# Kernel optimization log

Measured on AMD Instinct MI355X. Metric: run time of the kernel, lower is better.

Reference implementation:

```python
import jax, jax.numpy as jnp
import numpy as np

B = 131072

def _lin(x, w, b):
    return x @ w.T + b

def setup_inputs() -> dict:
    key = jax.random.key(0)
    ks = jax.random.split(key, 32)
    def rn(k, shape, scale=0.05):
        return jax.random.normal(k, shape, dtype=jnp.float32) * scale
    inp = {
        "x": rn(ks[0], (B, 256), 1.0),
        "w": rn(ks[1], (B, 36), 1.0),
        "h0": rn(ks[2], (B, 32), 1.0),
        "c0": rn(ks[3], (B, 32), 1.0),
        "fc1_w": rn(ks[4], (128, 256)), "fc1_b": rn(ks[5], (128,)),
        "fc1a_w": rn(ks[6], (128, 164)), "fc1a_b": rn(ks[7], (128,)),
        "fc1b_w": rn(ks[8], (128, 128)), "fc1b_b": rn(ks[9], (128,)),
        "w_game": rn(ks[10], (1, 12), 1.0),
        "fc1c_w": rn(ks[11], (64, 140)), "fc1c_b": rn(ks[12], (64,)),
        "fc2_w": rn(ks[13], (32, 64)), "fc2_b": rn(ks[14], (32,)),
        "fc3_w": rn(ks[15], (32, 32)), "fc3_b": rn(ks[16], (32,)),
        "w_ih": rn(ks[17], (128, 32)), "w_hh": rn(ks[18], (128, 32)),
        "b_ih": rn(ks[19], (128,)), "b_hh": rn(ks[20], (128,)),
        "fc4_w": rn(ks[21], (32, 32)), "fc4_b": rn(ks[22], (32,)),
        "fc5_w": rn(ks[23], (1, 32)), "fc5_b": rn(ks[24], (1,)),
    }
    return inp

def reference(x, w, h0, c0, fc1_w, fc1_b, fc1a_w, fc1a_b, fc1b_w, fc1b_b,
              w_game, fc1c_w, fc1c_b, fc2_w, fc2_b, fc3_w, fc3_b,
              w_ih, w_hh, b_ih, b_hh, fc4_w, fc4_b, fc5_w, fc5_b):
    b = x.shape[0]
    h = jax.nn.relu(_lin(x, fc1_w, fc1_b))                      # [B,128]
    h = jnp.concatenate([h, w], axis=-1)                        # [B,164]
    h = jax.nn.relu(_lin(h, fc1a_w, fc1a_b))                    # [B,128]
    h = jax.nn.relu(_lin(h, fc1b_w, fc1b_b))                    # [B,128]
    wg = jnp.broadcast_to(w_game.reshape(1, 12), (b, 12))
    h = jnp.concatenate([h, wg], axis=-1)                       # [B,140]
    h = jax.nn.relu(_lin(h, fc1c_w, fc1c_b))                    # [B,64]
    h = jax.nn.relu(_lin(h, fc2_w, fc2_b))                      # [B,32]
    h = jax.nn.relu(_lin(h, fc3_w, fc3_b))                      # [B,32]
    # LSTMCell step (torch gate order: input, forget, cell, output)
    gates = _lin(h, w_ih, b_ih) + _lin(h0, w_hh, b_hh)          # [B,128]
    i_g, f_g, g_g, o_g = jnp.split(gates, 4, axis=-1)
    c_new = jax.nn.sigmoid(f_g) * c0 + jax.nn.sigmoid(i_g) * jnp.tanh(g_g)
    h_new = jax.nn.sigmoid(o_g) * jnp.tanh(c_new)               # [B,32]
    out = jax.nn.relu(_lin(h_new, fc4_w, fc4_b))                # [B,32]
    out = _lin(out, fc5_w, fc5_b)                               # [B,1]
    return jax.nn.sigmoid(out)
```

## Files before the change

kernel.cpp:

```cpp
#include <hip/hip_runtime.h>
#include <hip/hip_bf16.h>


typedef __bf16 bf16x8 __attribute__((ext_vector_type(8)));
typedef float  f32x4  __attribute__((ext_vector_type(4)));
typedef int    i32x4  __attribute__((ext_vector_type(4)));

#define MFMA16(A, B, C) __builtin_amdgcn_mfma_f32_16x16x32_bf16((A), (B), (C), 0, 0, 0)

#define WOFF_FC1    0
#define WOFF_FC1A_H 32768
#define WOFF_FC1B   49152
#define WOFF_FC1C   65536
#define LDS_ELEMS   73728
#define WOFF_FC1A_W 73728
#define WOFF_FC2    81920
#define WOFF_FC3    83968
#define WOFF_WIH    84992
#define WOFF_WHH    89088
#define WOFF_FC4    93184
#define WTOT        94208
#define BOFF_FC1  0
#define BOFF_FC1A 128
#define BOFF_FC1B 256
#define BOFF_FC1C 384
#define BOFF_FC2  448
#define BOFF_FC3  480
#define BOFF_LSTM 512
#define BOFF_FC4  640
#define BTOT      672

__device__ __forceinline__ void conv_frag(int rel, const float* __restrict__ src,
                                          __bf16* __restrict__ dst,
                                          int ns, int Krow, int kbase, int klim, int perm) {
    int j    = rel & 7;
    int lane = (rel >> 3) & 63;
    int fs   = rel >> 9;
    int s    = fs % ns;
    int t    = fs / ns;
    int gq   = lane >> 4;
    int n    = 16 * t + (lane & 15);
    int k    = perm ? (16 * (2 * s + (j >> 2)) + 4 * gq + (j & 3))
                    : (32 * s + 8 * gq + j);
    float v  = (k < klim) ? src[n * Krow + kbase + k] : 0.f;
    dst[rel] = (__bf16)v;
}

__global__ void prep_kernel(const float* __restrict__ fc1w,  const float* __restrict__ fc1b,
                            const float* __restrict__ fc1aw, const float* __restrict__ fc1ab,
                            const float* __restrict__ fc1bw, const float* __restrict__ fc1bb,
                            const float* __restrict__ wgame, const float* __restrict__ fc1cw,
                            const float* __restrict__ fc1cb, const float* __restrict__ fc2w,
                            const float* __restrict__ fc2b,  const float* __restrict__ fc3w,
                            const float* __restrict__ fc3b,  const float* __restrict__ wih,
                            const float* __restrict__ whh,   const float* __restrict__ bih,
                            const float* __restrict__ bhh,   const float* __restrict__ fc4w,
                            const float* __restrict__ fc4b,
                            __bf16* __restrict__ wsw, float* __restrict__ wsb) {
    int idx = blockIdx.x * 256 + threadIdx.x;
    if (idx < WTOT) {
        if      (idx < WOFF_FC1A_H) conv_frag(idx - WOFF_FC1,    fc1w,  wsw + WOFF_FC1,    8, 256,   0, 256, 0);
        else if (idx < WOFF_FC1B)   conv_frag(idx - WOFF_FC1A_H, fc1aw, wsw + WOFF_FC1A_H, 4, 164,   0, 128, 1);
        else if (idx < WOFF_FC1C)   conv_frag(idx - WOFF_FC1B,   fc1bw, wsw + WOFF_FC1B,   4, 128,   0, 128, 1);
        else if (idx < WOFF_FC1A_W) conv_frag(idx - WOFF_FC1C,   fc1cw, wsw + WOFF_FC1C,   4, 140,   0, 128, 1);
        else if (idx < WOFF_FC2)    conv_frag(idx - WOFF_FC1A_W, fc1aw, wsw + WOFF_FC1A_W, 2, 164, 128,  36, 0);
        else if (idx < WOFF_FC3)    conv_frag(idx - WOFF_FC2,    fc2w,  wsw + WOFF_FC2,    2,  64,   0,  64, 1);
        else if (idx < WOFF_WIH)    conv_frag(idx - WOFF_FC3,    fc3w,  wsw + WOFF_FC3,    1,  32,   0,  32, 1);
        else if (idx < WOFF_WHH)    conv_frag(idx - WOFF_WIH,    wih,   wsw + WOFF_WIH,    1,  32,   0,  32, 1);
        else if (idx < WOFF_FC4)    conv_frag(idx - WOFF_WHH,    whh,   wsw + WOFF_WHH,    1,  32,   0,  32, 0);
        else                        conv_frag(idx - WOFF_FC4,    fc4w,  wsw + WOFF_FC4,    1,  32,   0,  32, 1);
    } else if (idx < WTOT + BTOT) {
        int bi = idx - WTOT;
        float v;
        if      (bi < 128) v = fc1b[bi];
        else if (bi < 256) v = fc1ab[bi - 128];
        else if (bi < 384) v = fc1bb[bi - 256];
        else if (bi < 448) {
            int n = bi - 384;
            v = fc1cb[n];
            for (int q = 0; q < 12; ++q) v += fc1cw[n * 140 + 128 + q] * wgame[q];
        }
        else if (bi < 480) v = fc2b[bi - 448];
        else if (bi < 512) v = fc3b[bi - 480];
        else if (bi < 640) { int n = bi - 512; v = bih[n] + bhh[n]; }
        else               v = fc4b[bi - 640];
        wsb[bi] = v;
    }
}

__device__ __forceinline__ bf16x8 ld8f(const float* __restrict__ p) {
    f32x4 a = *(const f32x4*)p;
    f32x4 b = *(const f32x4*)(p + 4);
    bf16x8 r;
    r[0] = (__bf16)a[0]; r[1] = (__bf16)a[1]; r[2] = (__bf16)a[2]; r[3] = (__bf16)a[3];
    r[4] = (__bf16)b[0]; r[5] = (__bf16)b[1]; r[6] = (__bf16)b[2]; r[7] = (__bf16)b[3];
    return r;
}

__device__ __forceinline__ bf16x8 ld4f_masked(const float* __restrict__ p, bool on) {
    f32x4 v = {0.f, 0.f, 0.f, 0.f};
    if (on) v = *(const f32x4*)p;
    bf16x8 r;
    r[0] = (__bf16)v[0]; r[1] = (__bf16)v[1]; r[2] = (__bf16)v[2]; r[3] = (__bf16)v[3];
    r[4] = (__bf16)0.f;  r[5] = (__bf16)0.f;  r[6] = (__bf16)0.f;  r[7] = (__bf16)0.f;
    return r;
}

__device__ __forceinline__ bf16x8 packrelu(const f32x4* a, int s) {
    bf16x8 r;
#pragma unroll
    for (int j = 0; j < 8; ++j) {
        float v = a[2 * s + (j >> 2)][j & 3];
        r[j] = (__bf16)fmaxf(v, 0.f);
    }
    return r;
}

__device__ __forceinline__ float sigm(float v)  { return 1.f / (1.f + __expf(-v)); }
__device__ __forceinline__ float tanh_(float v) { return 1.f - 2.f / (1.f + __expf(2.f * v)); }

__global__ __launch_bounds__(512, 2) void fused_mlp_lstm(
        const float* __restrict__ x,  const float* __restrict__ w,
        const float* __restrict__ h0, const float* __restrict__ c0,
        const float* __restrict__ fc5w, const float* __restrict__ fc5b,
        const __bf16* __restrict__ wsw, const float* __restrict__ wsb,
        float* __restrict__ out) {
    __shared__ __align__(16) __bf16 slds[LDS_ELEMS];

    const int tid     = threadIdx.x;
    const int lane    = tid & 63;
    const int wv      = blockIdx.x * 8 + (tid >> 6);
    const int gq      = lane >> 4;
    const int mr      = lane & 15;
    const int rowbase = wv * 32;
    const int row0    = rowbase + mr;
    const int row1    = rowbase + 16 + mr;

    {
        const i32x4* gs = (const i32x4*)wsw;
        i32x4*       sd = (i32x4*)slds;
#pragma unroll
        for (int i = 0; i < 18; ++i) sd[i * 512 + tid] = gs[i * 512 + tid];
    }

    bf16x8 xf[2][8];
#pragma unroll
    for (int s = 0; s < 8; ++s) {
        xf[0][s] = ld8f(x + row0 * 256 + 32 * s + 8 * gq);
        xf[1][s] = ld8f(x + row1 * 256 + 32 * s + 8 * gq);
    }
    bf16x8 wxa0 = ld8f(w + row0 * 36 + 8 * gq);
    bf16x8 wxb0 = ld8f(w + row1 * 36 + 8 * gq);
    bf16x8 wxa1 = ld4f_masked(w + row0 * 36 + 32, gq == 0);
    bf16x8 wxb1 = ld4f_masked(w + row1 * 36 + 32, gq == 0);

    __syncthreads();

    const bf16x8* Wfc1  = (const bf16x8*)(slds + WOFF_FC1);
    const bf16x8* Wf1aH = (const bf16x8*)(slds + WOFF_FC1A_H);
    const bf16x8* Wfc1b = (const bf16x8*)(slds + WOFF_FC1B);
    const bf16x8* Wfc1c = (const bf16x8*)(slds + WOFF_FC1C);
    const bf16x8* Wf1aW = (const bf16x8*)(wsw + WOFF_FC1A_W);
    const bf16x8* Wfc2  = (const bf16x8*)(wsw + WOFF_FC2);
    const bf16x8* Wfc3  = (const bf16x8*)(wsw + WOFF_FC3);
    const bf16x8* Wwih  = (const bf16x8*)(wsw + WOFF_WIH);
    const bf16x8* Wwhh  = (const bf16x8*)(wsw + WOFF_WHH);
    const bf16x8* Wfc4  = (const bf16x8*)(wsw + WOFF_FC4);

    f32x4 acc1[2][8];
#pragma unroll
    for (int t = 0; t < 8; ++t) {
        f32x4 bv = *(const f32x4*)(wsb + BOFF_FC1 + 16 * t + 4 * gq);
        acc1[0][t] = bv; acc1[1][t] = bv;
    }
#pragma unroll
    for (int s = 0; s < 8; ++s) {
#pragma unroll
        for (int t = 0; t < 8; ++t) {
            bf16x8 wf = Wfc1[(t * 8 + s) * 64 + lane];
            acc1[0][t] = MFMA16(wf, xf[0][s], acc1[0][t]);
            acc1[1][t] = MFMA16(wf, xf[1][s], acc1[1][t]);
        }
    }
    bf16x8 h0fa = ld8f(h0 + row0 * 32 + 8 * gq);
    bf16x8 h0fb = ld8f(h0 + row1 * 32 + 8 * gq);

    bf16x8 h1f[2][4];
#pragma unroll
    for (int s = 0; s < 4; ++s) { h1f[0][s] = packrelu(acc1[0], s); h1f[1][s] = packrelu(acc1[1], s); }

    f32x4 acc2[2][8];
#pragma unroll
    for (int t = 0; t < 8; ++t) {
        f32x4 bv = *(const f32x4*)(wsb + BOFF_FC1A + 16 * t + 4 * gq);
        acc2[0][t] = bv; acc2[1][t] = bv;
    }
#pragma unroll
    for (int s = 0; s < 4; ++s) {
#pragma unroll
        for (int t = 0; t < 8; ++t) {
            bf16x8 wf = Wf1aH[(t * 4 + s) * 64 + lane];
            acc2[0][t] = MFMA16(wf, h1f[0][s], acc2[0][t]);
            acc2[1][t] = MFMA16(wf, h1f[1][s], acc2[1][t]);
        }
    }
#pragma unroll
    for (int t = 0; t < 8; ++t) {
        bf16x8 wf0 = Wf1aW[(t * 2 + 0) * 64 + lane];
        bf16x8 wf1 = Wf1aW[(t * 2 + 1) * 64 + lane];
        acc2[0][t] = MFMA16(wf0, wxa0, acc2[0][t]);
        acc2[1][t] = MFMA16(wf0, wxb0, acc2[1][t]);
        acc2[0][t] = MFMA16(wf1, wxa1, acc2[0][t]);
        acc2[1][t] = MFMA16(wf1, wxb1, acc2[1][t]);
    }
    f32x4 c0r[2][2];
#pragma unroll
    for (int t2 = 0; t2 < 2; ++t2) {
        c0r[0][t2] = *(const f32x4*)(c0 + row0 * 32 + 16 * t2 + 4 * gq);
        c0r[1][t2] = *(const f32x4*)(c0 + row1 * 32 + 16 * t2 + 4 * gq);
    }

    bf16x8 h2f[2][4];
#pragma unroll
    for (int s = 0; s < 4; ++s) { h2f[0][s] = packrelu(acc2[0], s); h2f[1][s] = packrelu(acc2[1], s); }

    f32x4 acc3[2][8];
#pragma unroll
    for (int t = 0; t < 8; ++t) {
        f32x4 bv = *(const f32x4*)(wsb + BOFF_FC1B + 16 * t + 4 * gq);
        acc3[0][t] = bv; acc3[1][t] = bv;
    }
#pragma unroll
    for (int s = 0; s < 4; ++s) {
#pragma unroll
        for (int t = 0; t < 8; ++t) {
            bf16x8 wf = Wfc1b[(t * 4 + s) * 64 + lane];
            acc3[0][t] = MFMA16(wf, h2f[0][s], acc3[0][t]);
            acc3[1][t] = MFMA16(wf, h2f[1][s], acc3[1][t]);
        }
    }
    bf16x8 h3f[2][4];
#pragma unroll
    for (int s = 0; s < 4; ++s) { h3f[0][s] = packrelu(acc3[0], s); h3f[1][s] = packrelu(acc3[1], s); }

    f32x4 acc4[2][4];
#pragma unroll
    for (int t = 0; t < 4; ++t) {
        f32x4 bv = *(const f32x4*)(wsb + BOFF_FC1C + 16 * t + 4 * gq);
        acc4[0][t] = bv; acc4[1][t] = bv;
    }
#pragma unroll
    for (int s = 0; s < 4; ++s) {
#pragma unroll
        for (int t = 0; t < 4; ++t) {
            bf16x8 wf = Wfc1c[(t * 4 + s) * 64 + lane];
            acc4[0][t] = MFMA16(wf, h3f[0][s], acc4[0][t]);
            acc4[1][t] = MFMA16(wf, h3f[1][s], acc4[1][t]);
        }
    }
    bf16x8 h4f[2][2];
#pragma unroll
    for (int s = 0; s < 2; ++s) { h4f[0][s] = packrelu(acc4[0], s); h4f[1][s] = packrelu(acc4[1], s); }

    f32x4 acc5[2][2];
#pragma unroll
    for (int t = 0; t < 2; ++t) {
        f32x4 bv = *(const f32x4*)(wsb + BOFF_FC2 + 16 * t + 4 * gq);
        acc5[0][t] = bv; acc5[1][t] = bv;
    }
#pragma unroll
    for (int s = 0; s < 2; ++s) {
#pragma unroll
        for (int t = 0; t < 2; ++t) {
            bf16x8 wf = Wfc2[(t * 2 + s) * 64 + lane];
            acc5[0][t] = MFMA16(wf, h4f[0][s], acc5[0][t]);
            acc5[1][t] = MFMA16(wf, h4f[1][s], acc5[1][t]);
        }
    }
    bf16x8 h5f[2] = { packrelu(acc5[0], 0), packrelu(acc5[1], 0) };

    f32x4 acc6[2][2];
#pragma unroll
    for (int t = 0; t < 2; ++t) {
        f32x4 bv = *(const f32x4*)(wsb + BOFF_FC3 + 16 * t + 4 * gq);
        acc6[0][t] = bv; acc6[1][t] = bv;
    }
#pragma unroll
    for (int t = 0; t < 2; ++t) {
        bf16x8 wf = Wfc3[t * 64 + lane];
        acc6[0][t] = MFMA16(wf, h5f[0], acc6[0][t]);
        acc6[1][t] = MFMA16(wf, h5f[1], acc6[1][t]);
    }
    bf16x8 h6f[2] = { packrelu(acc6[0], 0), packrelu(acc6[1], 0) };

    f32x4 accg[2][8];
#pragma unroll
    for (int t = 0; t < 8; ++t) {
        f32x4 bv = *(const f32x4*)(wsb + BOFF_LSTM + 16 * t + 4 * gq);
        accg[0][t] = bv; accg[1][t] = bv;
    }
#pragma unroll
    for (int t = 0; t < 8; ++t) {
        bf16x8 wf = Wwih[t * 64 + lane];
        accg[0][t] = MFMA16(wf, h6f[0], accg[0][t]);
        accg[1][t] = MFMA16(wf, h6f[1], accg[1][t]);
    }
#pragma unroll
    for (int t = 0; t < 8; ++t) {
        bf16x8 wf = Wwhh[t * 64 + lane];
        accg[0][t] = MFMA16(wf, h0fa, accg[0][t]);
        accg[1][t] = MFMA16(wf, h0fb, accg[1][t]);
    }
    float hn[2][8];
#pragma unroll
    for (int m = 0; m < 2; ++m) {
#pragma unroll
        for (int t2 = 0; t2 < 2; ++t2) {
            f32x4 cc = c0r[m][t2];
#pragma unroll
            for (int r = 0; r < 4; ++r) {
                float ig = accg[m][t2][r];
                float fg = accg[m][2 + t2][r];
                float gg = accg[m][4 + t2][r];
                float og = accg[m][6 + t2][r];
                float cn = sigm(fg) * cc[r] + sigm(ig) * tanh_(gg);
                hn[m][t2 * 4 + r] = sigm(og) * tanh_(cn);
            }
        }
    }
    bf16x8 hnf[2];
#pragma unroll
    for (int m = 0; m < 2; ++m)
#pragma unroll
        for (int j = 0; j < 8; ++j) hnf[m][j] = (__bf16)hn[m][j];

    f32x4 acco[2][2];
#pragma unroll
    for (int t = 0; t < 2; ++t) {
        f32x4 bv = *(const f32x4*)(wsb + BOFF_FC4 + 16 * t + 4 * gq);
        acco[0][t] = bv; acco[1][t] = bv;
    }
#pragma unroll
    for (int t = 0; t < 2; ++t) {
        bf16x8 wf = Wfc4[t * 64 + lane];
        acco[0][t] = MFMA16(wf, hnf[0], acco[0][t]);
        acco[1][t] = MFMA16(wf, hnf[1], acco[1][t]);
    }

    f32x4 w5a = *(const f32x4*)(fc5w + 4 * gq);
    f32x4 w5b = *(const f32x4*)(fc5w + 16 + 4 * gq);
    float b5  = fc5b[0];
    float res[2];
#pragma unroll
    for (int m = 0; m < 2; ++m) {
        float p = 0.f;
#pragma unroll
        for (int r = 0; r < 4; ++r) {
            p += fmaxf(acco[m][0][r], 0.f) * w5a[r];
            p += fmaxf(acco[m][1][r], 0.f) * w5b[r];
        }
        p += __shfl_xor(p, 16);
        p += __shfl_xor(p, 32);
        res[m] = sigm(p + b5);
    }
    if (lane < 16) {
        out[rowbase + lane]      = res[0];
        out[rowbase + 16 + lane] = res[1];
    }
}

extern "C" void kernel_launch(void* const* d_in, const int* in_sizes, int n_in,
                              void* d_out, int out_size, void* d_ws, size_t ws_size,
                              hipStream_t stream) {
    const float* x     = (const float*)d_in[0];
    const float* w     = (const float*)d_in[1];
    const float* h0    = (const float*)d_in[2];
    const float* c0    = (const float*)d_in[3];
    const float* fc1w  = (const float*)d_in[4];
    const float* fc1b  = (const float*)d_in[5];
    const float* fc1aw = (const float*)d_in[6];
    const float* fc1ab = (const float*)d_in[7];
    const float* fc1bw = (const float*)d_in[8];
    const float* fc1bb = (const float*)d_in[9];
    const float* wgame = (const float*)d_in[10];
    const float* fc1cw = (const float*)d_in[11];
    const float* fc1cb = (const float*)d_in[12];
    const float* fc2w  = (const float*)d_in[13];
    const float* fc2b  = (const float*)d_in[14];
    const float* fc3w  = (const float*)d_in[15];
    const float* fc3b  = (const float*)d_in[16];
    const float* wih   = (const float*)d_in[17];
    const float* whh   = (const float*)d_in[18];
    const float* bih   = (const float*)d_in[19];
    const float* bhh   = (const float*)d_in[20];
    const float* fc4w  = (const float*)d_in[21];
    const float* fc4b  = (const float*)d_in[22];
    const float* fc5w  = (const float*)d_in[23];
    const float* fc5b  = (const float*)d_in[24];

    __bf16* wsw = (__bf16*)d_ws;
    float*  wsb = (float*)((char*)d_ws + WTOT * sizeof(__bf16));
    (void)ws_size; (void)n_in; (void)out_size;

    const int Btot = in_sizes[0] / 256;

    prep_kernel<<<(WTOT + BTOT + 255) / 256, 256, 0, stream>>>(
        fc1w, fc1b, fc1aw, fc1ab, fc1bw, fc1bb, wgame, fc1cw, fc1cb,
        fc2w, fc2b, fc3w, fc3b, wih, whh, bih, bhh, fc4w, fc4b, wsw, wsb);

    fused_mlp_lstm<<<Btot / 256, 512, 0, stream>>>(
        x, w, h0, c0, fc5w, fc5b, wsw, wsb, (float*)d_out);
}
```

Baseline: 64.32 us.

## Use 1024-thread blocks with 16-row waves processing two sequential row chunks

Each block grows to 1024 threads and covers 512 rows. Every wave now handles one 16-row MFMA tile at a time and loops over two chunks, instead of interleaving two 32-row tiles. The LDS weight staging is spread over more threads and more rows per block, and the lower register footprint per wave is meant to let twice as many waves fit on a CU under the same LDS limit. In exchange, each wave has less independent MFMA work to hide latency. The tighter launch bound may also cap registers hard enough to cause spills.

```diff
diff --git a/kernel.cpp b/kernel.cpp
--- a/kernel.cpp
+++ b/kernel.cpp
@@ -119,7 +119,7 @@
 __device__ __forceinline__ float sigm(float v)  { return 1.f / (1.f + __expf(-v)); }
 __device__ __forceinline__ float tanh_(float v) { return 1.f - 2.f / (1.f + __expf(2.f * v)); }
 
-__global__ __launch_bounds__(512, 2) void fused_mlp_lstm(
+__global__ __launch_bounds__(1024, 4) void fused_mlp_lstm(
         const float* __restrict__ x,  const float* __restrict__ w,
         const float* __restrict__ h0, const float* __restrict__ c0,
         const float* __restrict__ fc5w, const float* __restrict__ fc5b,
@@ -127,33 +127,22 @@
         float* __restrict__ out) {
     __shared__ __align__(16) __bf16 slds[LDS_ELEMS];
 
-    const int tid     = threadIdx.x;
-    const int lane    = tid & 63;
-    const int wv      = blockIdx.x * 8 + (tid >> 6);
-    const int gq      = lane >> 4;
-    const int mr      = lane & 15;
-    const int rowbase = wv * 32;
-    const int row0    = rowbase + mr;
-    const int row1    = rowbase + 16 + mr;
+    const int tid  = threadIdx.x;
+    const int lane = tid & 63;
+    const int gq   = lane >> 4;
+    const int mr   = lane & 15;
+    const int rowbase0 = blockIdx.x * 512 + (tid >> 6) * 16;
+
+    bf16x8 xf[8];
+#pragma unroll
+    for (int s = 0; s < 8; ++s) xf[s] = ld8f(x + (rowbase0 + mr) * 256 + 32 * s + 8 * gq);
 
     {
         const i32x4* gs = (const i32x4*)wsw;
         i32x4*       sd = (i32x4*)slds;
 #pragma unroll
-        for (int i = 0; i < 18; ++i) sd[i * 512 + tid] = gs[i * 512 + tid];
+        for (int i = 0; i < 9; ++i) sd[i * 1024 + tid] = gs[i * 1024 + tid];
     }
-
-    bf16x8 xf[2][8];
-#pragma unroll
-    for (int s = 0; s < 8; ++s) {
-        xf[0][s] = ld8f(x + row0 * 256 + 32 * s + 8 * gq);
-        xf[1][s] = ld8f(x + row1 * 256 + 32 * s + 8 * gq);
-    }
-    bf16x8 wxa0 = ld8f(w + row0 * 36 + 8 * gq);
-    bf16x8 wxb0 = ld8f(w + row1 * 36 + 8 * gq);
-    bf16x8 wxa1 = ld4f_masked(w + row0 * 36 + 32, gq == 0);
-    bf16x8 wxb1 = ld4f_masked(w + row1 * 36 + 32, gq == 0);
-
     __syncthreads();
 
     const bf16x8* Wfc1  = (const bf16x8*)(slds + WOFF_FC1);
@@ -167,205 +156,158 @@
     const bf16x8* Wwhh  = (const bf16x8*)(wsw + WOFF_WHH);
     const bf16x8* Wfc4  = (const bf16x8*)(wsw + WOFF_FC4);
 
-    f32x4 acc1[2][8];
-#pragma unroll
-    for (int t = 0; t < 8; ++t) {
-        f32x4 bv = *(const f32x4*)(wsb + BOFF_FC1 + 16 * t + 4 * gq);
-        acc1[0][t] = bv; acc1[1][t] = bv;
-    }
-#pragma unroll
-    for (int s = 0; s < 8; ++s) {
-#pragma unroll
-        for (int t = 0; t < 8; ++t) {
-            bf16x8 wf = Wfc1[(t * 8 + s) * 64 + lane];
-            acc1[0][t] = MFMA16(wf, xf[0][s], acc1[0][t]);
-            acc1[1][t] = MFMA16(wf, xf[1][s], acc1[1][t]);
-        }
-    }
-    bf16x8 h0fa = ld8f(h0 + row0 * 32 + 8 * gq);
-    bf16x8 h0fb = ld8f(h0 + row1 * 32 + 8 * gq);
-
-    bf16x8 h1f[2][4];
-#pragma unroll
-    for (int s = 0; s < 4; ++s) { h1f[0][s] = packrelu(acc1[0], s); h1f[1][s] = packrelu(acc1[1], s); }
-
-    f32x4 acc2[2][8];
-#pragma unroll
-    for (int t = 0; t < 8; ++t) {
-        f32x4 bv = *(const f32x4*)(wsb + BOFF_FC1A + 16 * t + 4 * gq);
-        acc2[0][t] = bv; acc2[1][t] = bv;
-    }
-#pragma unroll
-    for (int s = 0; s < 4; ++s) {
-#pragma unroll
-        for (int t = 0; t < 8; ++t) {
-            bf16x8 wf = Wf1aH[(t * 4 + s) * 64 + lane];
-            acc2[0][t] = MFMA16(wf, h1f[0][s], acc2[0][t]);
-            acc2[1][t] = MFMA16(wf, h1f[1][s], acc2[1][t]);
-        }
-    }
-#pragma unroll
-    for (int t = 0; t < 8; ++t) {
-        bf16x8 wf0 = Wf1aW[(t * 2 + 0) * 64 + lane];
-        bf16x8 wf1 = Wf1aW[(t * 2 + 1) * 64 + lane];
-        acc2[0][t] = MFMA16(wf0, wxa0, acc2[0][t]);
-        acc2[1][t] = MFMA16(wf0, wxb0, acc2[1][t]);
-        acc2[0][t] = MFMA16(wf1, wxa1, acc2[0][t]);
-        acc2[1][t] = MFMA16(wf1, wxb1, acc2[1][t]);
-    }
-    f32x4 c0r[2][2];
-#pragma unroll
-    for (int t2 = 0; t2 < 2; ++t2) {
-        c0r[0][t2] = *(const f32x4*)(c0 + row0 * 32 + 16 * t2 + 4 * gq);
-        c0r[1][t2] = *(const f32x4*)(c0 + row1 * 32 + 16 * t2 + 4 * gq);
-    }
-
-    bf16x8 h2f[2][4];
-#pragma unroll
-    for (int s = 0; s < 4; ++s) { h2f[0][s] = packrelu(acc2[0], s); h2f[1][s] = packrelu(acc2[1], s); }
-
-    f32x4 acc3[2][8];
-#pragma unroll
-    for (int t = 0; t < 8; ++t) {
-        f32x4 bv = *(const f32x4*)(wsb + BOFF_FC1B + 16 * t + 4 * gq);
-        acc3[0][t] = bv; acc3[1][t] = bv;
-    }
-#pragma unroll
-    for (int s = 0; s < 4; ++s) {
-#pragma unroll
-        for (int t = 0; t < 8; ++t) {
-            bf16x8 wf = Wfc1b[(t * 4 + s) * 64 + lane];
-            acc3[0][t] = MFMA16(wf, h2f[0][s], acc3[0][t]);
-            acc3[1][t] = MFMA16(wf, h2f[1][s], acc3[1][t]);
-        }
-    }
-    bf16x8 h3f[2][4];
-#pragma unroll
-    for (int s = 0; s < 4; ++s) { h3f[0][s] = packrelu(acc3[0], s); h3f[1][s] = packrelu(acc3[1], s); }
-
-    f32x4 acc4[2][4];
-#pragma unroll
-    for (int t = 0; t < 4; ++t) {
-        f32x4 bv = *(const f32x4*)(wsb + BOFF_FC1C + 16 * t + 4 * gq);
-        acc4[0][t] = bv; acc4[1][t] = bv;
-    }
-#pragma unroll
-    for (int s = 0; s < 4; ++s) {
-#pragma unroll
-        for (int t = 0; t < 4; ++t) {
-            bf16x8 wf = Wfc1c[(t * 4 + s) * 64 + lane];
-            acc4[0][t] = MFMA16(wf, h3f[0][s], acc4[0][t]);
-            acc4[1][t] = MFMA16(wf, h3f[1][s], acc4[1][t]);
-        }
-    }
-    bf16x8 h4f[2][2];
-#pragma unroll
-    for (int s = 0; s < 2; ++s) { h4f[0][s] = packrelu(acc4[0], s); h4f[1][s] = packrelu(acc4[1], s); }
-
-    f32x4 acc5[2][2];
-#pragma unroll
-    for (int t = 0; t < 2; ++t) {
-        f32x4 bv = *(const f32x4*)(wsb + BOFF_FC2 + 16 * t + 4 * gq);
-        acc5[0][t] = bv; acc5[1][t] = bv;
-    }
-#pragma unroll
-    for (int s = 0; s < 2; ++s) {
-#pragma unroll
-        for (int t = 0; t < 2; ++t) {
-            bf16x8 wf = Wfc2[(t * 2 + s) * 64 + lane];
-            acc5[0][t] = MFMA16(wf, h4f[0][s], acc5[0][t]);
-            acc5[1][t] = MFMA16(wf, h4f[1][s], acc5[1][t]);
-        }
-    }
-    bf16x8 h5f[2] = { packrelu(acc5[0], 0), packrelu(acc5[1], 0) };
-
-    f32x4 acc6[2][2];
-#pragma unroll
-    for (int t = 0; t < 2; ++t) {
-        f32x4 bv = *(const f32x4*)(wsb + BOFF_FC3 + 16 * t + 4 * gq);
-        acc6[0][t] = bv; acc6[1][t] = bv;
-    }
-#pragma unroll
-    for (int t = 0; t < 2; ++t) {
-        bf16x8 wf = Wfc3[t * 64 + lane];
-        acc6[0][t] = MFMA16(wf, h5f[0], acc6[0][t]);
-        acc6[1][t] = MFMA16(wf, h5f[1], acc6[1][t]);
-    }
-    bf16x8 h6f[2] = { packrelu(acc6[0], 0), packrelu(acc6[1], 0) };
-
-    f32x4 accg[2][8];
-#pragma unroll
-    for (int t = 0; t < 8; ++t) {
-        f32x4 bv = *(const f32x4*)(wsb + BOFF_LSTM + 16 * t + 4 * gq);
-        accg[0][t] = bv; accg[1][t] = bv;
-    }
-#pragma unroll
-    for (int t = 0; t < 8; ++t) {
-        bf16x8 wf = Wwih[t * 64 + lane];
-        accg[0][t] = MFMA16(wf, h6f[0], accg[0][t]);
-        accg[1][t] = MFMA16(wf, h6f[1], accg[1][t]);
-    }
-#pragma unroll
-    for (int t = 0; t < 8; ++t) {
-        bf16x8 wf = Wwhh[t * 64 + lane];
-        accg[0][t] = MFMA16(wf, h0fa, accg[0][t]);
-        accg[1][t] = MFMA16(wf, h0fb, accg[1][t]);
-    }
-    float hn[2][8];
-#pragma unroll
-    for (int m = 0; m < 2; ++m) {
-#pragma unroll
-        for (int t2 = 0; t2 < 2; ++t2) {
-            f32x4 cc = c0r[m][t2];
-#pragma unroll
-            for (int r = 0; r < 4; ++r) {
-                float ig = accg[m][t2][r];
-                float fg = accg[m][2 + t2][r];
-                float gg = accg[m][4 + t2][r];
-                float og = accg[m][6 + t2][r];
-                float cn = sigm(fg) * cc[r] + sigm(ig) * tanh_(gg);
-                hn[m][t2 * 4 + r] = sigm(og) * tanh_(cn);
+#pragma unroll
+    for (int chain = 0; chain < 2; ++chain) {
+        const int rowbase = rowbase0 + chain * 256;
+        const int row     = rowbase + mr;
+        if (chain) {
+#pragma unroll
+            for (int s = 0; s < 8; ++s) xf[s] = ld8f(x + row * 256 + 32 * s + 8 * gq);
+        }
+        bf16x8 wxa0 = ld8f(w + row * 36 + 8 * gq);
+        bf16x8 wxa1 = ld4f_masked(w + row * 36 + 32, gq == 0);
+        bf16x8 h0f  = ld8f(h0 + row * 32 + 8 * gq);
+        f32x4  c0r0 = *(const f32x4*)(c0 + row * 32 + 4 * gq);
+        f32x4  c0r1 = *(const f32x4*)(c0 + row * 32 + 16 + 4 * gq);
+
+        bf16x8 h1f[4];
+        {
+            f32x4 acc1[8];
+#pragma unroll
+            for (int t = 0; t < 8; ++t)
+                acc1[t] = *(const f32x4*)(wsb + BOFF_FC1 + 16 * t + 4 * gq);
+#pragma unroll
+            for (int s = 0; s < 8; ++s)
+#pragma unroll
+                for (int t = 0; t < 8; ++t)
+                    acc1[t] = MFMA16(Wfc1[(t * 8 + s) * 64 + lane], xf[s], acc1[t]);
+#pragma unroll
+            for (int s = 0; s < 4; ++s) h1f[s] = packrelu(acc1, s);
+        }
+
+        bf16x8 h2f[4];
+        {
+            f32x4 acc2[8];
+#pragma unroll
+            for (int t = 0; t < 8; ++t)
+                acc2[t] = *(const f32x4*)(wsb + BOFF_FC1A + 16 * t + 4 * gq);
+#pragma unroll
+            for (int s = 0; s < 4; ++s)
+#pragma unroll
+                for (int t = 0; t < 8; ++t)
+                    acc2[t] = MFMA16(Wf1aH[(t * 4 + s) * 64 + lane], h1f[s], acc2[t]);
+#pragma unroll
+            for (int t = 0; t < 8; ++t) {
+                acc2[t] = MFMA16(Wf1aW[(t * 2 + 0) * 64 + lane], wxa0, acc2[t]);
+                acc2[t] = MFMA16(Wf1aW[(t * 2 + 1) * 64 + lane], wxa1, acc2[t]);
             }
-        }
-    }
-    bf16x8 hnf[2];
-#pragma unroll
-    for (int m = 0; m < 2; ++m)
-#pragma unroll
-        for (int j = 0; j < 8; ++j) hnf[m][j] = (__bf16)hn[m][j];
-
-    f32x4 acco[2][2];
-#pragma unroll
-    for (int t = 0; t < 2; ++t) {
-        f32x4 bv = *(const f32x4*)(wsb + BOFF_FC4 + 16 * t + 4 * gq);
-        acco[0][t] = bv; acco[1][t] = bv;
-    }
-#pragma unroll
-    for (int t = 0; t < 2; ++t) {
-        bf16x8 wf = Wfc4[t * 64 + lane];
-        acco[0][t] = MFMA16(wf, hnf[0], acco[0][t]);
-        acco[1][t] = MFMA16(wf, hnf[1], acco[1][t]);
-    }
-
-    f32x4 w5a = *(const f32x4*)(fc5w + 4 * gq);
-    f32x4 w5b = *(const f32x4*)(fc5w + 16 + 4 * gq);
-    float b5  = fc5b[0];
-    float res[2];
-#pragma unroll
-    for (int m = 0; m < 2; ++m) {
+#pragma unroll
+            for (int s = 0; s < 4; ++s) h2f[s] = packrelu(acc2, s);
+        }
+
+        bf16x8 h3f[4];
+        {
+            f32x4 acc3[8];
+#pragma unroll
+            for (int t = 0; t < 8; ++t)
+                acc3[t] = *(const f32x4*)(wsb + BOFF_FC1B + 16 * t + 4 * gq);
+#pragma unroll
+            for (int s = 0; s < 4; ++s)
+#pragma unroll
+                for (int t = 0; t < 8; ++t)
+                    acc3[t] = MFMA16(Wfc1b[(t * 4 + s) * 64 + lane], h2f[s], acc3[t]);
+#pragma unroll
+            for (int s = 0; s < 4; ++s) h3f[s] = packrelu(acc3, s);
+        }
+
+        bf16x8 h4f[2];
+        {
+            f32x4 acc4[4];
+#pragma unroll
+            for (int t = 0; t < 4; ++t)
+                acc4[t] = *(const f32x4*)(wsb + BOFF_FC1C + 16 * t + 4 * gq);
+#pragma unroll
+            for (int s = 0; s < 4; ++s)
+#pragma unroll
+                for (int t = 0; t < 4; ++t)
+                    acc4[t] = MFMA16(Wfc1c[(t * 4 + s) * 64 + lane], h3f[s], acc4[t]);
+#pragma unroll
+            for (int s = 0; s < 2; ++s) h4f[s] = packrelu(acc4, s);
+        }
+
+        bf16x8 h5f;
+        {
+            f32x4 acc5[2];
+#pragma unroll
+            for (int t = 0; t < 2; ++t)
+                acc5[t] = *(const f32x4*)(wsb + BOFF_FC2 + 16 * t + 4 * gq);
+#pragma unroll
+            for (int s = 0; s < 2; ++s)
+#pragma unroll
+                for (int t = 0; t < 2; ++t)
+                    acc5[t] = MFMA16(Wfc2[(t * 2 + s) * 64 + lane], h4f[s], acc5[t]);
+            h5f = packrelu(acc5, 0);
+        }
+
+        bf16x8 h6f;
+        {
+            f32x4 acc6[2];
+#pragma unroll
+            for (int t = 0; t < 2; ++t)
+                acc6[t] = *(const f32x4*)(wsb + BOFF_FC3 + 16 * t + 4 * gq);
+#pragma unroll
+            for (int t = 0; t < 2; ++t)
+                acc6[t] = MFMA16(Wfc3[t * 64 + lane], h5f, acc6[t]);
+            h6f = packrelu(acc6, 0);
+        }
+
+        bf16x8 hnf;
+        {
+            f32x4 accg[8];
+#pragma unroll
+            for (int t = 0; t < 8; ++t)
+                accg[t] = *(const f32x4*)(wsb + BOFF_LSTM + 16 * t + 4 * gq);
+#pragma unroll
+            for (int t = 0; t < 8; ++t)
+                accg[t] = MFMA16(Wwih[t * 64 + lane], h6f, accg[t]);
+#pragma unroll
+            for (int t = 0; t < 8; ++t)
+                accg[t] = MFMA16(Wwhh[t * 64 + lane], h0f, accg[t]);
+#pragma unroll
+            for (int t2 = 0; t2 < 2; ++t2) {
+                f32x4 cc = t2 ? c0r1 : c0r0;
+#pragma unroll
+                for (int r = 0; r < 4; ++r) {
+                    float ig = accg[t2][r];
+                    float fg = accg[2 + t2][r];
+                    float gg = accg[4 + t2][r];
+                    float og = accg[6 + t2][r];
+                    float cn = sigm(fg) * cc[r] + sigm(ig) * tanh_(gg);
+                    hnf[t2 * 4 + r] = (__bf16)(sigm(og) * tanh_(cn));
+                }
+            }
+        }
+
+        f32x4 acco[2];
+#pragma unroll
+        for (int t = 0; t < 2; ++t)
+            acco[t] = *(const f32x4*)(wsb + BOFF_FC4 + 16 * t + 4 * gq);
+#pragma unroll
+        for (int t = 0; t < 2; ++t)
+            acco[t] = MFMA16(Wfc4[t * 64 + lane], hnf, acco[t]);
+
+        f32x4 w5a = *(const f32x4*)(fc5w + 4 * gq);
+        f32x4 w5b = *(const f32x4*)(fc5w + 16 + 4 * gq);
         float p = 0.f;
 #pragma unroll
         for (int r = 0; r < 4; ++r) {
-            p += fmaxf(acco[m][0][r], 0.f) * w5a[r];
-            p += fmaxf(acco[m][1][r], 0.f) * w5b[r];
+            p += fmaxf(acco[0][r], 0.f) * w5a[r];
+            p += fmaxf(acco[1][r], 0.f) * w5b[r];
         }
         p += __shfl_xor(p, 16);
         p += __shfl_xor(p, 32);
-        res[m] = sigm(p + b5);
-    }
-    if (lane < 16) {
-        out[rowbase + lane]      = res[0];
-        out[rowbase + 16 + lane] = res[1];
+        float res = sigm(p + fc5b[0]);
+        if (lane < 16) out[rowbase + lane] = res;
     }
 }
 
@@ -408,6 +350,6 @@
         fc1w, fc1b, fc1aw, fc1ab, fc1bw, fc1bb, wgame, fc1cw, fc1cb,
         fc2w, fc2b, fc3w, fc3b, wih, whh, bih, bhh, fc4w, fc4b, wsw, wsb);
 
-    fused_mlp_lstm<<<Btot / 256, 512, 0, stream>>>(
+    fused_mlp_lstm<<<Btot / 512, 1024, 0, stream>>>(
         x, w, h0, c0, fc5w, fc5b, wsw, wsb, (float*)d_out);
 }
```

Result: slower. 91.88 us (+42.8%).
